# Performance work log

Hardware: AMD Instinct MI355X
Metric: run time of the kernel (lower is better)

## Reference

```python
import jax, jax.numpy as jnp
import numpy as np

HEADS = 8
DIM_HEAD = 32
SCALE = DIM_HEAD ** -0.5
EPS = 1e-5


def setup_inputs() -> dict:
    key = jax.random.key(0)
    ks = jax.random.split(key, 4)
    b, dim, l = 8, 256, 16384
    hidden = HEADS * DIM_HEAD  # 256
    x = jax.random.normal(ks[0], (b, dim, l), dtype=jnp.float32)
    w_qkv = jax.random.normal(ks[1], (hidden * 3, dim), dtype=jnp.float32) * (dim ** -0.5)
    w_out = jax.random.normal(ks[2], (dim, hidden), dtype=jnp.float32) * (hidden ** -0.5)
    b_out = jax.random.normal(ks[3], (dim,), dtype=jnp.float32) * 0.02
    gn_w = jnp.ones((dim,), dtype=jnp.float32)
    gn_b = jnp.zeros((dim,), dtype=jnp.float32)
    return {"x": x, "w_qkv": w_qkv, "w_out": w_out, "b_out": b_out,
            "gn_w": gn_w, "gn_b": gn_b}


def reference(x, w_qkv, w_out, b_out, gn_w, gn_b):
    b, c, l = x.shape
    h, d = HEADS, DIM_HEAD
    # 1x1 conv == channel matmul: [3*hidden, c] x [b, c, l] -> [b, 3*hidden, l]
    qkv = jnp.einsum('oc,bcl->bol', w_qkv, x)
    q, k, v = jnp.split(qkv, 3, axis=1)
    # b (h d) l -> b h d l
    q = q.reshape(b, h, d, l)
    k = k.reshape(b, h, d, l)
    v = v.reshape(b, h, d, l)
    q = jax.nn.softmax(q, axis=2) * SCALE  # softmax over per-head channel dim
    k = jax.nn.softmax(k, axis=3)          # softmax over sequence length
    context = jnp.einsum('bhdn,bhen->bhde', k, v)
    out = jnp.einsum('bhde,bhdn->bhen', context, q)  # [b, h, e, l]
    out = out.reshape(b, h * d, l)
    # output 1x1 conv with bias
    out = jnp.einsum('oc,bcl->bol', w_out, out) + b_out[None, :, None]
    # GroupNorm(1, dim): normalize over (C, L) per batch element
    mean = jnp.mean(out, axis=(1, 2), keepdims=True)
    var = jnp.var(out, axis=(1, 2), keepdims=True)
    out = (out - mean) * jax.lax.rsqrt(var + EPS)
    return out * gn_w[None, :, None] + gn_b[None, :, None]
```

## Files before the change

### kernel.cpp

```cpp
#include <hip/hip_runtime.h>
#include <hip/hip_bf16.h>
#include <cstdint>
#include <cstddef>


#define NB 8
#define NC 256
#define NL 16384
#define NH 8
#define ND 32
#define NO3 768

#define Q_SCALE 0.17677669529663687f
#define GN_EPS 1e-5f

using f32x4  = __attribute__((ext_vector_type(4))) float;
using bf16x8 = __attribute__((ext_vector_type(8))) __bf16;
using u32x4  = __attribute__((ext_vector_type(4))) unsigned int;

__device__ __forceinline__ float bf2f(unsigned short u) {
    union { unsigned int i; float f; } v; v.i = ((unsigned int)u) << 16; return v.f;
}
__device__ __forceinline__ unsigned short f2bf(float f) {
    union { float f; unsigned int i; } v; v.f = f;
    v.i += 0x7fffu + ((v.i >> 16) & 1u);
    return (unsigned short)(v.i >> 16);
}
__device__ __forceinline__ bf16x8 ldfrag(const unsigned short* p) {
    return __builtin_bit_cast(bf16x8, *(const u32x4*)p);
}

__global__ __launch_bounds__(256) void k_init(
    const float* __restrict__ wqkv, unsigned short* __restrict__ wq,
    float* __restrict__ ctx, float* __restrict__ Zs, float* __restrict__ stats)
{
    const int i0 = blockIdx.x * 256 + threadIdx.x;
    const int stride = gridDim.x * 256;
    for (int i = i0; i < NO3 * NC; i += stride) wq[i] = f2bf(wqkv[i]);
    for (int i = i0; i < NB * NH * ND * ND; i += stride) ctx[i] = 0.f;
    for (int i = i0; i < NB * NC; i += stride) Zs[i] = 0.f;
    if (i0 < 16) stats[i0] = 0.f;
}

__global__ __launch_bounds__(512) void k_qkv(
    const float* __restrict__ x, const unsigned short* __restrict__ wq,
    unsigned short* __restrict__ q_ws, float* __restrict__ ctx, float* __restrict__ Zs)
{
    __shared__ __align__(16) unsigned short xT[64 * 256];
    __shared__ __align__(16) unsigned short qkv[NO3 * 72];

    const int b    = blockIdx.y;
    const int l0   = blockIdx.x << 6;
    const int tid  = threadIdx.x;
    const int lane = tid & 63;
    const int w    = tid >> 6;
    const int m    = lane & 15;
    const int g    = lane >> 4;

    {
        const int l = lane;
        #pragma unroll 8
        for (int p = 0; p < 32; ++p) {
            const int c = w + (p << 3);
            const float v = x[((size_t)(b * NC + c) << 14) + l0 + l];
            xT[(l * 256 + c) ^ ((l & 7) << 3)] = f2bf(v);
        }
    }
    __syncthreads();

    f32x4 acc[6][4];
    #pragma unroll
    for (int i = 0; i < 6; ++i) {
        #pragma unroll
        for (int j = 0; j < 4; ++j) acc[i][j] = f32x4{0.f, 0.f, 0.f, 0.f};
    }
    #pragma unroll
    for (int ks = 0; ks < 8; ++ks) {
        bf16x8 afr[6], bfr[4];
        #pragma unroll
        for (int rt = 0; rt < 6; ++rt)
            afr[rt] = ldfrag(wq + ((96 * w + 16 * rt + m) << 8) + (ks << 5) + (g << 3));
        #pragma unroll
        for (int ct = 0; ct < 4; ++ct) {
            const int col = (ct << 4) + m;
            bfr[ct] = ldfrag(xT + ((col * 256 + (ks << 5) + (g << 3)) ^ ((col & 7) << 3)));
        }
        #pragma unroll
        for (int rt = 0; rt < 6; ++rt) {
            #pragma unroll
            for (int ct = 0; ct < 4; ++ct)
                acc[rt][ct] = __builtin_amdgcn_mfma_f32_16x16x32_bf16(
                    afr[rt], bfr[ct], acc[rt][ct], 0, 0, 0);
        }
    }

    #pragma unroll
    for (int rt = 0; rt < 6; ++rt) {
        #pragma unroll
        for (int ct = 0; ct < 4; ++ct) {
            #pragma unroll
            for (int r = 0; r < 4; ++r)
                qkv[(96 * w + 16 * rt + 4 * g + r) * 72 + (ct << 4) + m] =
                    f2bf(acc[rt][ct][r]);
        }
    }
    __syncthreads();

    {
        const int h = w, cc = lane;
        float vq[32];
        float s = 0.f;
        #pragma unroll
        for (int d = 0; d < 32; ++d) {
            const float f = __expf(bf2f(qkv[(32 * h + d) * 72 + cc]));
            vq[d] = f; s += f;
        }
        const float rs = Q_SCALE / s;
        unsigned short* qp = q_ws + ((size_t)(b * NC + 32 * h) << 14) + l0 + cc;
        #pragma unroll
        for (int d = 0; d < 32; ++d) qp[(size_t)d << 14] = f2bf(vq[d] * rs);
    }

    {
        const int row = tid >> 1, half = tid & 1;
        unsigned short* kp = qkv + (NC + row) * 72 + (half << 5);
        float s = 0.f;
        #pragma unroll
        for (int j = 0; j < 32; ++j) {
            const unsigned short ub = f2bf(__expf(bf2f(kp[j])));
            kp[j] = ub;
            s += bf2f(ub);
        }
        s += __shfl_xor(s, 1);
        if (half == 0) atomicAdd(Zs + b * NC + row, s);
    }
    __syncthreads();

    {
        const int h = w;
        f32x4 ca[2][2];
        #pragma unroll
        for (int i = 0; i < 2; ++i) { ca[i][0] = f32x4{0.f,0.f,0.f,0.f}; ca[i][1] = f32x4{0.f,0.f,0.f,0.f}; }
        #pragma unroll
        for (int ks = 0; ks < 2; ++ks) {
            bf16x8 ea[2], vb[2];
            #pragma unroll
            for (int t = 0; t < 2; ++t) {
                ea[t] = ldfrag(qkv + (NC     + 32 * h + 16 * t + m) * 72 + (ks << 5) + (g << 3));
                vb[t] = ldfrag(qkv + (2 * NC + 32 * h + 16 * t + m) * 72 + (ks << 5) + (g << 3));
            }
            #pragma unroll
            for (int mt = 0; mt < 2; ++mt) {
                #pragma unroll
                for (int nt = 0; nt < 2; ++nt)
                    ca[mt][nt] = __builtin_amdgcn_mfma_f32_16x16x32_bf16(
                        ea[mt], vb[nt], ca[mt][nt], 0, 0, 0);
            }
        }
        float* cbase = ctx + ((b * NH + h) << 10);
        #pragma unroll
        for (int mt = 0; mt < 2; ++mt) {
            #pragma unroll
            for (int nt = 0; nt < 2; ++nt) {
                #pragma unroll
                for (int r = 0; r < 4; ++r)
                    atomicAdd(cbase + ((16 * mt + 4 * g + r) << 5) + (nt << 4) + m,
                              ca[mt][nt][r]);
            }
        }
    }
}

__global__ __launch_bounds__(256) void k_w2(
    const float* __restrict__ w_out, const float* __restrict__ ctx,
    const float* __restrict__ Zs, unsigned short* __restrict__ W2)
{
    const int b = blockIdx.y, o = blockIdx.x, c = threadIdx.x;
    const int h = c >> 5, d = c & 31;
    const float zinv = 1.f / Zs[b * NC + c];
    const float* wrow = w_out + (o << 8) + (h << 5);
    const float* crow = ctx + ((b * NH + h) << 10) + (d << 5);
    float s = 0.f;
    #pragma unroll
    for (int e = 0; e < 32; ++e) s += wrow[e] * crow[e];
    W2[((size_t)(b * NC + o) << 8) + c] = f2bf(s * zinv);
}

__global__ __launch_bounds__(512) void k_out(
    const unsigned short* __restrict__ q_ws, const unsigned short* __restrict__ W2,
    const float* __restrict__ b_out, float* __restrict__ y, float* __restrict__ stats)
{
    __shared__ __align__(16) unsigned short qT[128 * 256];
    __shared__ float red[16];

    const int b    = blockIdx.y;
    const int l0   = blockIdx.x << 7;
    const int tid  = threadIdx.x;
    const int lane = tid & 63, w = tid >> 6, m = lane & 15, g = lane >> 4;

    {
        const int l = tid & 127, c0 = tid >> 7;
        const unsigned short* qp = q_ws + ((size_t)b << 22) + l0 + l;
        #pragma unroll 16
        for (int p = 0; p < 64; ++p) {
            const int c = c0 + (p << 2);
            qT[(l * 256 + c) ^ ((l & 7) << 3)] = qp[(size_t)c << 14];
        }
    }
    __syncthreads();

    const unsigned short* W2b = W2 + ((size_t)b << 16);
    f32x4 acc[2][8];
    #pragma unroll
    for (int i = 0; i < 2; ++i) {
        #pragma unroll
        for (int j = 0; j < 8; ++j) acc[i][j] = f32x4{0.f, 0.f, 0.f, 0.f};
    }
    #pragma unroll
    for (int ks = 0; ks < 8; ++ks) {
        bf16x8 afr[2], bfr[8];
        #pragma unroll
        for (int rt = 0; rt < 2; ++rt)
            afr[rt] = ldfrag(W2b + ((32 * w + 16 * rt + m) << 8) + (ks << 5) + (g << 3));
        #pragma unroll
        for (int ct = 0; ct < 8; ++ct) {
            const int col = (ct << 4) + m;
            bfr[ct] = ldfrag(qT + ((col * 256 + (ks << 5) + (g << 3)) ^ ((col & 7) << 3)));
        }
        #pragma unroll
        for (int rt = 0; rt < 2; ++rt) {
            #pragma unroll
            for (int ct = 0; ct < 8; ++ct)
                acc[rt][ct] = __builtin_amdgcn_mfma_f32_16x16x32_bf16(
                    afr[rt], bfr[ct], acc[rt][ct], 0, 0, 0);
        }
    }

    float lsum = 0.f, lsq = 0.f;
    #pragma unroll
    for (int rt = 0; rt < 2; ++rt) {
        #pragma unroll
        for (int r = 0; r < 4; ++r) {
            const int row = 32 * w + 16 * rt + 4 * g + r;
            const float bo = b_out[row];
            float* yp = y + ((size_t)(b * NC + row) << 14) + l0 + m;
            #pragma unroll
            for (int ct = 0; ct < 8; ++ct) {
                const float v = acc[rt][ct][r] + bo;
                yp[ct << 4] = v;
                lsum += v; lsq += v * v;
            }
        }
    }
    #pragma unroll
    for (int off = 32; off > 0; off >>= 1) {
        lsum += __shfl_xor(lsum, off);
        lsq  += __shfl_xor(lsq,  off);
    }
    if (lane == 0) { red[w] = lsum; red[8 + w] = lsq; }
    __syncthreads();
    if (tid == 0) {
        float s = 0.f, s2 = 0.f;
        #pragma unroll
        for (int i = 0; i < 8; ++i) { s += red[i]; s2 += red[8 + i]; }
        atomicAdd(stats + b, s);
        atomicAdd(stats + 8 + b, s2);
    }
}

__global__ __launch_bounds__(64) void k_stats(const float* __restrict__ stats,
                                              float* __restrict__ sc)
{
    const int b = threadIdx.x;
    if (b < 8) {
        const float invN = 1.f / 4194304.f;
        const float mean = stats[b] * invN;
        const float var  = stats[8 + b] * invN - mean * mean;
        const float inv  = rsqrtf(var + GN_EPS);
        sc[b] = inv;
        sc[8 + b] = -mean * inv;
    }
}

__global__ __launch_bounds__(256) void k_norm(float* __restrict__ y,
    const float* __restrict__ sc, const float* __restrict__ gw, const float* __restrict__ gb)
{
    const size_t n4 = (size_t)NB * NC * NL / 4;
    for (size_t i = (size_t)blockIdx.x * 256 + threadIdx.x; i < n4;
         i += (size_t)gridDim.x * 256) {
        const size_t idx = i << 2;
        const int b = (int)(idx >> 22);
        const int c = (int)(idx >> 14) & 255;
        float4 v = ((float4*)y)[i];
        const float A  = sc[b] * gw[c];
        const float Bc = sc[8 + b] * gw[c] + gb[c];
        v.x = v.x * A + Bc; v.y = v.y * A + Bc;
        v.z = v.z * A + Bc; v.w = v.w * A + Bc;
        ((float4*)y)[i] = v;
    }
}

extern "C" void kernel_launch(void* const* d_in, const int* in_sizes, int n_in,
                              void* d_out, int out_size, void* d_ws, size_t ws_size,
                              hipStream_t stream)
{
    (void)in_sizes; (void)n_in; (void)out_size; (void)ws_size;
    const float* x     = (const float*)d_in[0];
    const float* w_qkv = (const float*)d_in[1];
    const float* w_out = (const float*)d_in[2];
    const float* b_out = (const float*)d_in[3];
    const float* gn_w  = (const float*)d_in[4];
    const float* gn_b  = (const float*)d_in[5];
    float* out = (float*)d_out;

    char* ws = (char*)d_ws;
    unsigned short* q_ws = (unsigned short*)(ws);
    unsigned short* wq   = (unsigned short*)(ws + 67108864);
    unsigned short* W2   = (unsigned short*)(ws + 67502080);
    float* ctx   = (float*)(ws + 68550656);
    float* Zs    = (float*)(ws + 68812800);
    float* stats = (float*)(ws + 68820992);
    float* sc    = (float*)(ws + 68821056);

    k_init <<<dim3(256),          dim3(256), 0, stream>>>(w_qkv, wq, ctx, Zs, stats);
    k_qkv  <<<dim3(NL / 64, NB),  dim3(512), 0, stream>>>(x, wq, q_ws, ctx, Zs);
    k_w2   <<<dim3(NC, NB),       dim3(256), 0, stream>>>(w_out, ctx, Zs, W2);
    k_out  <<<dim3(NL / 128, NB), dim3(512), 0, stream>>>(q_ws, W2, b_out, out, stats);
    k_stats<<<dim3(1),            dim3(64),  0, stream>>>(stats, sc);
    k_norm <<<dim3(2048),         dim3(256), 0, stream>>>(out, sc, gn_w, gn_b);
}
```

Baseline: 289.0 us.

## Make QKV kernel persistent over chunks with double-buffered x and register-resident softmax

The QKV projection kernel now processes 8 consecutive 64-column chunks per block. While computing the current chunk it prefetches the next chunk of x into registers and stores it into a second LDS buffer. Each wave's rows are remapped so one wave holds q, k and v for its own head. That lets the q softmax and k exp run directly on the accumulators without staging the full qkv tile in LDS. Context and Z partial sums stay in registers across chunks, so global atomics are issued once per block instead of once per chunk. The cost is fewer blocks (256 instead of 2048) and higher register pressure, which may reduce occupancy and latency hiding.

```diff
diff --git a/kernel.cpp b/kernel.cpp
--- a/kernel.cpp
+++ b/kernel.cpp
@@ -10,6 +10,7 @@
 #define NH 8
 #define ND 32
 #define NO3 768
+#define CHUNKS 8
 
 #define Q_SCALE 0.17677669529663687f
 #define GN_EPS 1e-5f
@@ -46,127 +47,172 @@
     const float* __restrict__ x, const unsigned short* __restrict__ wq,
     unsigned short* __restrict__ q_ws, float* __restrict__ ctx, float* __restrict__ Zs)
 {
-    __shared__ __align__(16) unsigned short xT[64 * 256];
-    __shared__ __align__(16) unsigned short qkv[NO3 * 72];
+    __shared__ __align__(16) unsigned short xT[2][64 * 256];
+    __shared__ __align__(16) unsigned short ekv[8][2][32 * 72];
 
     const int b    = blockIdx.y;
-    const int l0   = blockIdx.x << 6;
+    const int lb   = blockIdx.x * (64 * CHUNKS);
     const int tid  = threadIdx.x;
     const int lane = tid & 63;
     const int w    = tid >> 6;
     const int m    = lane & 15;
     const int g    = lane >> 4;
 
+    const float* xb = x + ((size_t)b << 22);
+
+    f32x4 ca[2][2];
+    #pragma unroll
+    for (int i = 0; i < 2; ++i) {
+        #pragma unroll
+        for (int j = 0; j < 2; ++j) ca[i][j] = f32x4{0.f, 0.f, 0.f, 0.f};
+    }
+    float zacc[8] = {0.f,0.f,0.f,0.f,0.f,0.f,0.f,0.f};
+
     {
-        const int l = lane;
-        #pragma unroll 8
-        for (int p = 0; p < 32; ++p) {
-            const int c = w + (p << 3);
-            const float v = x[((size_t)(b * NC + c) << 14) + l0 + l];
-            xT[(l * 256 + c) ^ ((l & 7) << 3)] = f2bf(v);
+        #pragma unroll
+        for (int p = 0; p < 16; ++p) {
+            const int cp = w + (p << 3);
+            const float v0 = xb[((size_t)(2 * cp)     << 14) + lb + lane];
+            const float v1 = xb[((size_t)(2 * cp + 1) << 14) + lb + lane];
+            const unsigned int pk =
+                (unsigned int)f2bf(v0) | ((unsigned int)f2bf(v1) << 16);
+            *(unsigned int*)&xT[0][(((lane) << 8) + 2 * cp) ^ ((lane & 7) << 3)] = pk;
         }
     }
     __syncthreads();
 
-    f32x4 acc[6][4];
-    #pragma unroll
-    for (int i = 0; i < 6; ++i) {
-        #pragma unroll
-        for (int j = 0; j < 4; ++j) acc[i][j] = f32x4{0.f, 0.f, 0.f, 0.f};
-    }
-    #pragma unroll
-    for (int ks = 0; ks < 8; ++ks) {
-        bf16x8 afr[6], bfr[4];
-        #pragma unroll
-        for (int rt = 0; rt < 6; ++rt)
-            afr[rt] = ldfrag(wq + ((96 * w + 16 * rt + m) << 8) + (ks << 5) + (g << 3));
+    for (int t = 0; t < CHUNKS; ++t) {
+        const int l0 = lb + (t << 6);
+        const unsigned short* xcur = xT[t & 1];
+        const bool pf = (t + 1 < CHUNKS);
+
+        float sv0[16], sv1[16];
+        if (pf) {
+            #pragma unroll
+            for (int p = 0; p < 16; ++p) {
+                const int cp = w + (p << 3);
+                sv0[p] = xb[((size_t)(2 * cp)     << 14) + l0 + 64 + lane];
+                sv1[p] = xb[((size_t)(2 * cp + 1) << 14) + l0 + 64 + lane];
+            }
+        }
+
+        f32x4 acc[6][4];
+        #pragma unroll
+        for (int i = 0; i < 6; ++i) {
+            #pragma unroll
+            for (int j = 0; j < 4; ++j) acc[i][j] = f32x4{0.f, 0.f, 0.f, 0.f};
+        }
+        #pragma unroll
+        for (int ks = 0; ks < 8; ++ks) {
+            bf16x8 afr[6], bfr[4];
+            #pragma unroll
+            for (int rt = 0; rt < 6; ++rt) {
+                const int rb = ((rt >> 1) << 8) + 32 * w + ((rt & 1) << 4);
+                afr[rt] = ldfrag(wq + ((size_t)(rb + m) << 8) + (ks << 5) + (g << 3));
+            }
+            #pragma unroll
+            for (int ct = 0; ct < 4; ++ct)
+                bfr[ct] = ldfrag(&xcur[(((((ct << 4) + m) << 8) + (ks << 5) + (g << 3))
+                                        ^ ((m & 7) << 3))]);
+            #pragma unroll
+            for (int rt = 0; rt < 6; ++rt) {
+                #pragma unroll
+                for (int ct = 0; ct < 4; ++ct)
+                    acc[rt][ct] = __builtin_amdgcn_mfma_f32_16x16x32_bf16(
+                        afr[rt], bfr[ct], acc[rt][ct], 0, 0, 0);
+            }
+        }
+
+        float rs[4];
         #pragma unroll
         for (int ct = 0; ct < 4; ++ct) {
-            const int col = (ct << 4) + m;
-            bfr[ct] = ldfrag(xT + ((col * 256 + (ks << 5) + (g << 3)) ^ ((col & 7) << 3)));
-        }
-        #pragma unroll
-        for (int rt = 0; rt < 6; ++rt) {
-            #pragma unroll
-            for (int ct = 0; ct < 4; ++ct)
-                acc[rt][ct] = __builtin_amdgcn_mfma_f32_16x16x32_bf16(
-                    afr[rt], bfr[ct], acc[rt][ct], 0, 0, 0);
-        }
-    }
-
-    #pragma unroll
-    for (int rt = 0; rt < 6; ++rt) {
-        #pragma unroll
-        for (int ct = 0; ct < 4; ++ct) {
+            float s = 0.f;
+            #pragma unroll
+            for (int rt = 0; rt < 2; ++rt) {
+                #pragma unroll
+                for (int r = 0; r < 4; ++r) {
+                    const float e = __expf(acc[rt][ct][r]);
+                    acc[rt][ct][r] = e; s += e;
+                }
+            }
+            s += __shfl_xor(s, 16);
+            s += __shfl_xor(s, 32);
+            rs[ct] = Q_SCALE / s;
+        }
+        {
+            unsigned short* qb = q_ws + ((size_t)(b * NC + 32 * w) << 14) + l0;
+            #pragma unroll
+            for (int rt = 0; rt < 2; ++rt) {
+                #pragma unroll
+                for (int r = 0; r < 4; ++r) {
+                    const size_t ro = (size_t)(16 * rt + 4 * g + r) << 14;
+                    #pragma unroll
+                    for (int ct = 0; ct < 4; ++ct)
+                        qb[ro + (ct << 4) + m] = f2bf(acc[rt][ct][r] * rs[ct]);
+                }
+            }
+        }
+
+        unsigned short* eb = &ekv[w][0][0];
+        unsigned short* vv = &ekv[w][1][0];
+        #pragma unroll
+        for (int rt = 0; rt < 2; ++rt) {
+            #pragma unroll
+            for (int r = 0; r < 4; ++r) {
+                const int dl = 16 * rt + 4 * g + r;
+                #pragma unroll
+                for (int ct = 0; ct < 4; ++ct) {
+                    const unsigned short ue = f2bf(__expf(acc[2 + rt][ct][r]));
+                    zacc[4 * rt + r] += bf2f(ue);
+                    eb[dl * 72 + (ct << 4) + m] = ue;
+                    vv[dl * 72 + (ct << 4) + m] = f2bf(acc[4 + rt][ct][r]);
+                }
+            }
+        }
+
+        #pragma unroll
+        for (int ks = 0; ks < 2; ++ks) {
+            const int co = (ks << 5) + (g << 3);
+            bf16x8 ea0 = ldfrag(eb + m * 72 + co);
+            bf16x8 ea1 = ldfrag(eb + (16 + m) * 72 + co);
+            bf16x8 vb0 = ldfrag(vv + m * 72 + co);
+            bf16x8 vb1 = ldfrag(vv + (16 + m) * 72 + co);
+            ca[0][0] = __builtin_amdgcn_mfma_f32_16x16x32_bf16(ea0, vb0, ca[0][0], 0,0,0);
+            ca[0][1] = __builtin_amdgcn_mfma_f32_16x16x32_bf16(ea0, vb1, ca[0][1], 0,0,0);
+            ca[1][0] = __builtin_amdgcn_mfma_f32_16x16x32_bf16(ea1, vb0, ca[1][0], 0,0,0);
+            ca[1][1] = __builtin_amdgcn_mfma_f32_16x16x32_bf16(ea1, vb1, ca[1][1], 0,0,0);
+        }
+
+        if (pf) {
+            unsigned short* xn = xT[(t + 1) & 1];
+            #pragma unroll
+            for (int p = 0; p < 16; ++p) {
+                const int cp = w + (p << 3);
+                const unsigned int pk =
+                    (unsigned int)f2bf(sv0[p]) | ((unsigned int)f2bf(sv1[p]) << 16);
+                *(unsigned int*)&xn[(((lane) << 8) + 2 * cp) ^ ((lane & 7) << 3)] = pk;
+            }
+        }
+        __syncthreads();
+    }
+
+    #pragma unroll
+    for (int i = 0; i < 8; ++i) {
+        float z = zacc[i];
+        z += __shfl_xor(z, 1); z += __shfl_xor(z, 2);
+        z += __shfl_xor(z, 4); z += __shfl_xor(z, 8);
+        if (m == 0)
+            atomicAdd(Zs + b * NC + 32 * w + ((i >> 2) << 4) + 4 * g + (i & 3), z);
+    }
+    float* cb = ctx + ((size_t)(b * NH + w) << 10);
+    #pragma unroll
+    for (int mt = 0; mt < 2; ++mt) {
+        #pragma unroll
+        for (int nt = 0; nt < 2; ++nt) {
             #pragma unroll
             for (int r = 0; r < 4; ++r)
-                qkv[(96 * w + 16 * rt + 4 * g + r) * 72 + (ct << 4) + m] =
-                    f2bf(acc[rt][ct][r]);
-        }
-    }
-    __syncthreads();
-
-    {
-        const int h = w, cc = lane;
-        float vq[32];
-        float s = 0.f;
-        #pragma unroll
-        for (int d = 0; d < 32; ++d) {
-            const float f = __expf(bf2f(qkv[(32 * h + d) * 72 + cc]));
-            vq[d] = f; s += f;
-        }
-        const float rs = Q_SCALE / s;
-        unsigned short* qp = q_ws + ((size_t)(b * NC + 32 * h) << 14) + l0 + cc;
-        #pragma unroll
-        for (int d = 0; d < 32; ++d) qp[(size_t)d << 14] = f2bf(vq[d] * rs);
-    }
-
-    {
-        const int row = tid >> 1, half = tid & 1;
-        unsigned short* kp = qkv + (NC + row) * 72 + (half << 5);
-        float s = 0.f;
-        #pragma unroll
-        for (int j = 0; j < 32; ++j) {
-            const unsigned short ub = f2bf(__expf(bf2f(kp[j])));
-            kp[j] = ub;
-            s += bf2f(ub);
-        }
-        s += __shfl_xor(s, 1);
-        if (half == 0) atomicAdd(Zs + b * NC + row, s);
-    }
-    __syncthreads();
-
-    {
-        const int h = w;
-        f32x4 ca[2][2];
-        #pragma unroll
-        for (int i = 0; i < 2; ++i) { ca[i][0] = f32x4{0.f,0.f,0.f,0.f}; ca[i][1] = f32x4{0.f,0.f,0.f,0.f}; }
-        #pragma unroll
-        for (int ks = 0; ks < 2; ++ks) {
-            bf16x8 ea[2], vb[2];
-            #pragma unroll
-            for (int t = 0; t < 2; ++t) {
-                ea[t] = ldfrag(qkv + (NC     + 32 * h + 16 * t + m) * 72 + (ks << 5) + (g << 3));
-                vb[t] = ldfrag(qkv + (2 * NC + 32 * h + 16 * t + m) * 72 + (ks << 5) + (g << 3));
-            }
-            #pragma unroll
-            for (int mt = 0; mt < 2; ++mt) {
-                #pragma unroll
-                for (int nt = 0; nt < 2; ++nt)
-                    ca[mt][nt] = __builtin_amdgcn_mfma_f32_16x16x32_bf16(
-                        ea[mt], vb[nt], ca[mt][nt], 0, 0, 0);
-            }
-        }
-        float* cbase = ctx + ((b * NH + h) << 10);
-        #pragma unroll
-        for (int mt = 0; mt < 2; ++mt) {
-            #pragma unroll
-            for (int nt = 0; nt < 2; ++nt) {
-                #pragma unroll
-                for (int r = 0; r < 4; ++r)
-                    atomicAdd(cbase + ((16 * mt + 4 * g + r) << 5) + (nt << 4) + m,
-                              ca[mt][nt][r]);
-            }
+                atomicAdd(cb + (((mt << 4) + 4 * g + r) << 5) + (nt << 4) + m,
+                          ca[mt][nt][r]);
         }
     }
 }
@@ -322,10 +368,10 @@
     float* stats = (float*)(ws + 68820992);
     float* sc    = (float*)(ws + 68821056);
 
-    k_init <<<dim3(256),          dim3(256), 0, stream>>>(w_qkv, wq, ctx, Zs, stats);
-    k_qkv  <<<dim3(NL / 64, NB),  dim3(512), 0, stream>>>(x, wq, q_ws, ctx, Zs);
-    k_w2   <<<dim3(NC, NB),       dim3(256), 0, stream>>>(w_out, ctx, Zs, W2);
-    k_out  <<<dim3(NL / 128, NB), dim3(512), 0, stream>>>(q_ws, W2, b_out, out, stats);
-    k_stats<<<dim3(1),            dim3(64),  0, stream>>>(stats, sc);
-    k_norm <<<dim3(2048),         dim3(256), 0, stream>>>(out, sc, gn_w, gn_b);
-}
+    k_init <<<dim3(256),                    dim3(256), 0, stream>>>(w_qkv, wq, ctx, Zs, stats);
+    k_qkv  <<<dim3(NL / (64 * CHUNKS), NB), dim3(512), 0, stream>>>(x, wq, q_ws, ctx, Zs);
+    k_w2   <<<dim3(NC, NB),                 dim3(256), 0, stream>>>(w_out, ctx, Zs, W2);
+    k_out  <<<dim3(NL / 128, NB),           dim3(512), 0, stream>>>(q_ws, W2, b_out, out, stats);
+    k_stats<<<dim3(1),                      dim3(64),  0, stream>>>(stats, sc);
+    k_norm <<<dim3(2048),                   dim3(256), 0, stream>>>(out, sc, gn_w, gn_b);
+}
```

New measurement: 588.0 us. 2.03x slower.
